# Kernel optimization log

Measured on AMD Instinct MI355X. Metric: run time of the kernel, lower is better.

Reference implementation:

```python
import jax, jax.numpy as jnp
import numpy as np

TOP_K = 2
LN_EPS = 1e-6


def setup_inputs() -> dict:
    key = jax.random.key(0)
    ks = jax.random.split(key, 8)
    B, T, D, FF, E = 4, 512, 1024, 4096, 8
    x = jax.random.normal(ks[0], (B, T, D), dtype=jnp.float32)
    gate_w = jax.random.normal(ks[1], (E, D), dtype=jnp.float32) * (1.0 / np.sqrt(D))
    ln_g = jnp.ones((E, D), dtype=jnp.float32)
    ln_b = jnp.zeros((E, D), dtype=jnp.float32)
    w1 = jax.random.normal(ks[2], (E, FF, D), dtype=jnp.float32) * (1.0 / np.sqrt(D))
    b1 = jnp.zeros((E, FF), dtype=jnp.float32)
    w2 = jax.random.normal(ks[3], (E, D, FF), dtype=jnp.float32) * (1.0 / np.sqrt(FF))
    b2 = jnp.zeros((E, D), dtype=jnp.float32)
    return {"x": x, "gate_w": gate_w, "ln_g": ln_g, "ln_b": ln_b,
            "w1": w1, "b1": b1, "w2": w2, "b2": b2}


def reference(x, gate_w, ln_g, ln_b, w1, b1, w2, b2):
    B, T, D = x.shape
    E = gate_w.shape[0]
    N = B * T
    xf = x.reshape(N, D)

    # ---- Router: linear gate -> softmax -> top-k dispatch mask + aux loss ----
    logits = xf @ gate_w.T                          # [N, E]
    scores = jax.nn.softmax(logits, axis=-1)        # [N, E]
    topk_vals, topk_idx = jax.lax.top_k(scores, TOP_K)
    dispatch = jnp.zeros_like(scores).at[
        jnp.arange(N)[:, None], topk_idx].set(1.0)  # [N, E] 0/1 mask
    load = dispatch.sum(axis=0)                     # [E]
    importance = scores.sum(axis=0)                 # [E]
    aux_loss = (importance * load).sum() * E / (N * N)

    # ---- Experts (PositionwiseFeedForward, kernel_size=1, skip connection) ----
    # Dense-all-experts compute, masked combine: identical math to the
    # per-expert gather/scatter loop in the torch module.
    mu = xf.mean(axis=-1, keepdims=True)
    var = ((xf - mu) ** 2).mean(axis=-1, keepdims=True)
    norm = (xf - mu) / jnp.sqrt(var + LN_EPS)       # [N, D]
    xe = norm[:, None, :] * ln_g[None] + ln_b[None] # [N, E, D] per-expert LN
    h = jax.nn.relu(jnp.einsum('ned,efd->nef', xe, w1) + b1[None])  # [N, E, FF]
    y = jnp.einsum('nef,edf->ned', h, w2) + b2[None] + xf[:, None, :]  # +skip

    comb = scores * dispatch                        # top-k gate weights [N, E]
    out = jnp.einsum('ne,ned->nd', comb, y).reshape(B, T, D)
    return out, aux_loss
```

## Files before the change

kernel.cpp:

```cpp
#include <hip/hip_runtime.h>
#include <hip/hip_bf16.h>

#define N_TOK 2048
#define DMODEL 1024
#define NEXP 8
#define FFDIM 4096
#define NMAX 2048
#define PADROWS 5120
#define TMAX 40

#define BM 128
#define BN 128
#define BK 64
#define KSPL 4

typedef __attribute__((ext_vector_type(8))) short s16x8;
typedef __attribute__((ext_vector_type(4))) float f32x4;

__device__ __forceinline__ float bf2f(ushort u) {
    union { uint i; float f; } x; x.i = ((uint)u) << 16; return x.f;
}
__device__ __forceinline__ ushort f2bf(float f) {
    union { float f; uint i; } x; x.f = f;
    uint r = x.i + 0x7fffu + ((x.i >> 16) & 1u);
    return (ushort)(r >> 16);
}

__device__ __forceinline__ void gl_lds16(const void* g, void* l) {
    __builtin_amdgcn_global_load_lds(
        (const __attribute__((address_space(1))) unsigned int*)g,
        (__attribute__((address_space(3))) unsigned int*)l, 16, 0, 0);
}

__device__ __forceinline__ float block_sum(float v, float* s4) {
    #pragma unroll
    for (int off = 32; off; off >>= 1) v += __shfl_down(v, off);
    __syncthreads();
    if ((threadIdx.x & 63) == 0) s4[threadIdx.x >> 6] = v;
    __syncthreads();
    return s4[0] + s4[1] + s4[2] + s4[3];
}

__global__ __launch_bounds__(256)
void router_kernel(const float* __restrict__ x, const float* __restrict__ gate_w,
                   ushort* __restrict__ norm, float* __restrict__ scores,
                   int* __restrict__ cnt, int* __restrict__ lists,
                   int4* __restrict__ info, float2* __restrict__ gpair) {
    __shared__ float s4[4];
    const int n = blockIdx.x, tid = threadIdx.x;
    const float* xr = x + (size_t)n * DMODEL;
    float4 v = *(const float4*)(xr + tid * 4);

    float tot = block_sum(v.x + v.y + v.z + v.w, s4);
    float mu = tot * (1.0f / DMODEL);
    float d0 = v.x - mu, d1 = v.y - mu, d2 = v.z - mu, d3 = v.w - mu;
    float var = block_sum(d0 * d0 + d1 * d1 + d2 * d2 + d3 * d3, s4) * (1.0f / DMODEL);
    float rstd = rsqrtf(var + 1e-6f);

    ushort nb[4] = { f2bf(d0 * rstd), f2bf(d1 * rstd), f2bf(d2 * rstd), f2bf(d3 * rstd) };
    *(uint2*)(norm + (size_t)n * DMODEL + tid * 4) = *(uint2*)nb;

    float lg[NEXP];
    #pragma unroll
    for (int e = 0; e < NEXP; ++e) {
        float4 g = *(const float4*)(gate_w + (size_t)e * DMODEL + tid * 4);
        lg[e] = v.x * g.x + v.y * g.y + v.z * g.z + v.w * g.w;
    }
    #pragma unroll
    for (int e = 0; e < NEXP; ++e) lg[e] = block_sum(lg[e], s4);

    if (tid == 0) {
        float m = lg[0];
        #pragma unroll
        for (int e = 1; e < NEXP; ++e) m = fmaxf(m, lg[e]);
        float ex[NEXP], Z = 0.f;
        #pragma unroll
        for (int e = 0; e < NEXP; ++e) { ex[e] = expf(lg[e] - m); Z += ex[e]; }
        float inv = 1.0f / Z;
        float sc[NEXP];
        #pragma unroll
        for (int e = 0; e < NEXP; ++e) { sc[e] = ex[e] * inv; scores[n * NEXP + e] = sc[e]; }
        int i1 = 0;
        #pragma unroll
        for (int e = 1; e < NEXP; ++e) if (sc[e] > sc[i1]) i1 = e;
        int i2 = (i1 == 0) ? 1 : 0;
        #pragma unroll
        for (int e = 0; e < NEXP; ++e) if (e != i1 && sc[e] > sc[i2]) i2 = e;
        int s1 = atomicAdd(&cnt[i1], 1);
        lists[i1 * NMAX + s1] = n;
        int s2 = atomicAdd(&cnt[i2], 1);
        lists[i2 * NMAX + s2] = n;
        info[n] = make_int4(i1, s1, i2, s2);
        gpair[n] = make_float2(sc[i1], sc[i2]);
    }
}

__global__ __launch_bounds__(256)
void prep_kernel(const float* __restrict__ scores, const int* __restrict__ cnt,
                 int* __restrict__ offs_pad, int* __restrict__ ntiles,
                 int4* __restrict__ tilemap, float* __restrict__ aux_out) {
    __shared__ float s4[4];
    __shared__ float imp[NEXP];
    float part[NEXP] = {};
    for (int i = threadIdx.x; i < N_TOK; i += 256) {
        #pragma unroll
        for (int e = 0; e < NEXP; ++e) part[e] += scores[i * NEXP + e];
    }
    #pragma unroll
    for (int e = 0; e < NEXP; ++e) {
        float s = block_sum(part[e], s4);
        if (threadIdx.x == 0) imp[e] = s;
    }
    __syncthreads();
    if (threadIdx.x == 0) {
        float aux = 0.f; int pad = 0, idx = 0;
        #pragma unroll
        for (int e = 0; e < NEXP; ++e) {
            aux += imp[e] * (float)cnt[e];
            offs_pad[e] = pad;
            int tiles = (cnt[e] + BM - 1) / BM;
            for (int t = 0; t < tiles; ++t)
                tilemap[idx++] = make_int4(e, pad + t * BM, 0, 0);
            pad += tiles * BM;
        }
        offs_pad[NEXP] = pad;
        ntiles[0] = idx;
        aux_out[0] = aux * (float)NEXP / ((float)N_TOK * (float)N_TOK);
    }
}

__global__ __launch_bounds__(256)
void gather_kernel(const ushort* __restrict__ norm, const float* __restrict__ ln_g,
                   const float* __restrict__ ln_b, const int* __restrict__ offs_pad,
                   const int* __restrict__ cnt, const int* __restrict__ lists,
                   ushort* __restrict__ A1) {
    const int r = blockIdx.x;
    int e = 0;
    #pragma unroll
    for (int k = 1; k < NEXP; ++k) if (r >= offs_pad[k]) e = k;
    const int slot = r - offs_pad[e];
    const int t4 = threadIdx.x * 4;
    if (slot >= cnt[e]) {
        ushort z[4] = {};
        *(uint2*)(A1 + (size_t)r * DMODEL + t4) = *(uint2*)z;
        return;
    }
    const int token = lists[e * NMAX + slot];
    uint2 nbv = *(const uint2*)(norm + (size_t)token * DMODEL + t4);
    ushort ns[4]; *(uint2*)ns = nbv;
    float4 gv = *(const float4*)(ln_g + (size_t)e * DMODEL + t4);
    float4 bv = *(const float4*)(ln_b + (size_t)e * DMODEL + t4);
    ushort ob[4] = { f2bf(bf2f(ns[0]) * gv.x + bv.x), f2bf(bf2f(ns[1]) * gv.y + bv.y),
                     f2bf(bf2f(ns[2]) * gv.z + bv.z), f2bf(bf2f(ns[3]) * gv.w + bv.w) };
    *(uint2*)(A1 + (size_t)r * DMODEL + t4) = *(uint2*)ob;
}

template<int KDIM, int NT, int KSPLT, bool RELU>
__global__ __launch_bounds__(256, 2)
void moe_gemm(const ushort* __restrict__ A, const float* __restrict__ W,
              const float* __restrict__ bias, const int* __restrict__ ntiles,
              const int4* __restrict__ tilemap, ushort* __restrict__ hout,
              float* __restrict__ yout) {
    __shared__ ushort As[2][BM * BK];
    __shared__ ushort Ws[2][BN * BK];
    constexpr int NOUT = NT * BN;

    const int q = (int)gridDim.x >> 3;
    const int logical = ((int)blockIdx.x & 7) * q + ((int)blockIdx.x >> 3);
    const int bt = logical % TMAX;
    int g = logical / TMAX;
    if (bt >= ntiles[0]) return;
    const int nt = g % NT;
    const int kb = g / NT;
    const int4 tm = tilemap[bt];
    const int e = tm.x, row0 = tm.y;

    const int tid = threadIdx.x, lane = tid & 63, wave = tid >> 6;
    const int wm = (wave & 1) * 64, wn = (wave >> 1) * 64;
    const int trow = lane >> 3;
    const int scol = ((lane & 7) ^ trow) * 8;

    const ushort* Agb = A + (size_t)row0 * KDIM;
    const float*  Wgb = W + ((size_t)e * NOUT + nt * BN) * KDIM;

    f32x4 acc[4][4] = {};
    float4 wr[8];

    auto stageA = [&](int step, int b) {
        #pragma unroll
        for (int i = 0; i < 4; ++i) {
            int c = wave * 4 + i;
            gl_lds16(Agb + (size_t)(c * 8 + trow) * KDIM + step * BK + scol, &As[b][c * 512]);
        }
    };
    auto loadWreg = [&](int step) {
        #pragma unroll
        for (int i = 0; i < 4; ++i) {
            int c = tid + 256 * i;
            const float* p = Wgb + (size_t)(c >> 3) * KDIM + step * BK + (c & 7) * 8;
            wr[2 * i]     = *(const float4*)p;
            wr[2 * i + 1] = *(const float4*)(p + 4);
        }
    };
    auto cvtWriteW = [&](int b) {
        #pragma unroll
        for (int i = 0; i < 4; ++i) {
            int c = tid + 256 * i;
            int row = c >> 3, col8 = (c & 7) * 8;
            union { s16x8 v; __hip_bfloat162 h2[4]; } u;
            u.h2[0] = __float22bfloat162_rn(make_float2(wr[2 * i].x, wr[2 * i].y));
            u.h2[1] = __float22bfloat162_rn(make_float2(wr[2 * i].z, wr[2 * i].w));
            u.h2[2] = __float22bfloat162_rn(make_float2(wr[2 * i + 1].x, wr[2 * i + 1].y));
            u.h2[3] = __float22bfloat162_rn(make_float2(wr[2 * i + 1].z, wr[2 * i + 1].w));
            *(s16x8*)&Ws[b][row * BK + (col8 ^ ((row & 7) << 3))] = u.v;
        }
    };
    auto mfma_phase = [&](int b) {
        #pragma unroll
        for (int kki = 0; kki < 2; ++kki) {
            const int cx = (kki * 32 + (lane >> 4) * 8) ^ ((lane & 7) << 3);
            s16x8 af[4], bfv[4];
            #pragma unroll
            for (int mi = 0; mi < 4; ++mi)
                af[mi] = *(const s16x8*)&As[b][(wm + mi * 16 + (lane & 15)) * BK + cx];
            #pragma unroll
            for (int ni = 0; ni < 4; ++ni)
                bfv[ni] = *(const s16x8*)&Ws[b][(wn + ni * 16 + (lane & 15)) * BK + cx];
            #pragma unroll
            for (int mi = 0; mi < 4; ++mi)
                #pragma unroll
                for (int ni = 0; ni < 4; ++ni)
                    acc[mi][ni] = __builtin_amdgcn_mfma_f32_16x16x32_bf16(
                        af[mi], bfv[ni], acc[mi][ni], 0, 0, 0);
        }
    };

    const int KS = KDIM / BK / KSPLT;
    const int kt0 = kb * KS;

    loadWreg(kt0);
    stageA(kt0, 0);
    cvtWriteW(0);
    __syncthreads();

    int buf = 0;
    for (int s = 0; s < KS; ++s) {
        if (s + 1 < KS) {
            stageA(kt0 + s + 1, buf ^ 1);
            loadWreg(kt0 + s + 1);
        }
        mfma_phase(buf);
        if (s + 1 < KS) cvtWriteW(buf ^ 1);
        __syncthreads();
        buf ^= 1;
    }

    if (RELU) {
        #pragma unroll
        for (int ni = 0; ni < 4; ++ni) {
            const int nn = nt * BN + wn + ni * 16 + (lane & 15);
            const float bv = bias[(size_t)e * NOUT + nn];
            #pragma unroll
            for (int mi = 0; mi < 4; ++mi)
                #pragma unroll
                for (int r = 0; r < 4; ++r) {
                    const int sl = wm + mi * 16 + ((lane >> 4) << 2) + r;
                    hout[(size_t)(row0 + sl) * NOUT + nn] =
                        f2bf(fmaxf(acc[mi][ni][r] + bv, 0.f));
                }
        }
    } else {
        #pragma unroll
        for (int ni = 0; ni < 4; ++ni) {
            const int nn = nt * BN + wn + ni * 16 + (lane & 15);
            #pragma unroll
            for (int mi = 0; mi < 4; ++mi)
                #pragma unroll
                for (int r = 0; r < 4; ++r) {
                    const int sl = wm + mi * 16 + ((lane >> 4) << 2) + r;
                    yout[((size_t)kb * PADROWS + row0 + sl) * NOUT + nn] = acc[mi][ni][r];
                }
        }
    }
}

__global__ __launch_bounds__(256)
void combine_kernel(const float* __restrict__ ypart, const float* __restrict__ b2,
                    const float* __restrict__ x, const int* __restrict__ offs_pad,
                    const int4* __restrict__ info, const float2* __restrict__ gpair,
                    float* __restrict__ out) {
    const int n = blockIdx.x, d = threadIdx.x * 4;
    const int4 ii = info[n];
    const float2 g = gpair[n];
    const int r1 = offs_pad[ii.x] + ii.y, r2 = offs_pad[ii.z] + ii.w;
    f32x4 y1 = {}, y2 = {};
    #pragma unroll
    for (int kb = 0; kb < KSPL; ++kb) {
        y1 += *(const f32x4*)(ypart + ((size_t)kb * PADROWS + r1) * DMODEL + d);
        y2 += *(const f32x4*)(ypart + ((size_t)kb * PADROWS + r2) * DMODEL + d);
    }
    const f32x4 b21 = *(const f32x4*)(b2 + (size_t)ii.x * DMODEL + d);
    const f32x4 b22 = *(const f32x4*)(b2 + (size_t)ii.z * DMODEL + d);
    const f32x4 xv  = *(const f32x4*)(x + (size_t)n * DMODEL + d);
    f32x4 o = g.x * (y1 + b21 + xv) + g.y * (y2 + b22 + xv);
    *(f32x4*)(out + (size_t)n * DMODEL + d) = o;
}

extern "C" void kernel_launch(void* const* d_in, const int* in_sizes, int n_in,
                              void* d_out, int out_size, void* d_ws, size_t ws_size,
                              hipStream_t stream) {
    const float* x      = (const float*)d_in[0];
    const float* gate_w = (const float*)d_in[1];
    const float* ln_g   = (const float*)d_in[2];
    const float* ln_b   = (const float*)d_in[3];
    const float* w1     = (const float*)d_in[4];
    const float* b1     = (const float*)d_in[5];
    const float* w2     = (const float*)d_in[6];
    const float* b2     = (const float*)d_in[7];
    float* out = (float*)d_out;

    char* w = (char*)d_ws;
    int*    cnt      = (int*)(w + 0);
    int*    offs_pad = (int*)(w + 64);
    int*    ntiles   = (int*)(w + 128);
    int4*   tilemap  = (int4*)(w + 192);
    int*    lists    = (int*)(w + 1024);
    float*  scores   = (float*)(w + 66560);
    int4*   info     = (int4*)(w + 132096);
    float2* gpair    = (float2*)(w + 164864);
    ushort* norm     = (ushort*)(w + 181248);
    ushort* A1       = (ushort*)(w + 4375552);
    ushort* h        = (ushort*)(w + 14861312);
    float*  ypart    = (float*)(w + 56804352);

    hipMemsetAsync(cnt, 0, 64, stream);

    router_kernel<<<N_TOK, 256, 0, stream>>>(x, gate_w, norm, scores, cnt, lists, info, gpair);
    prep_kernel<<<1, 256, 0, stream>>>(scores, cnt, offs_pad, ntiles, tilemap,
                                       out + (size_t)N_TOK * DMODEL);
    gather_kernel<<<PADROWS, 256, 0, stream>>>(norm, ln_g, ln_b, offs_pad, cnt, lists, A1);
    moe_gemm<DMODEL, FFDIM / BN, 1, true><<<TMAX * (FFDIM / BN), 256, 0, stream>>>(
        A1, w1, b1, ntiles, tilemap, h, nullptr);
    moe_gemm<FFDIM, DMODEL / BN, KSPL, false><<<TMAX * (DMODEL / BN) * KSPL, 256, 0, stream>>>(
        h, w2, nullptr, ntiles, tilemap, nullptr, ypart);
    combine_kernel<<<N_TOK, 256, 0, stream>>>(ypart, b2, x, offs_pad, info, gpair, out);
}
```

Baseline: 309.9 us.

## Drop LDS double buffering and raise occupancy target in MoE GEMM

Replaces the double-buffered LDS pipeline with a single buffer. Each k-step now loads A and W, converts W, syncs, runs the MFMAs and syncs again. Launch bounds go from 2 to 4 blocks per CU, relying on more resident blocks to hide latency instead of in-kernel prefetch. This halves LDS use per block, but it loses load/compute overlap within a block and adds a second barrier per step. The tighter register budget may also cause spills given the 64 fp32 accumulators and W staging registers.

```diff
diff --git a/kernel.cpp b/kernel.cpp
--- a/kernel.cpp
+++ b/kernel.cpp
@@ -156,13 +156,13 @@
 }
 
 template<int KDIM, int NT, int KSPLT, bool RELU>
-__global__ __launch_bounds__(256, 2)
+__global__ __launch_bounds__(256, 4)
 void moe_gemm(const ushort* __restrict__ A, const float* __restrict__ W,
               const float* __restrict__ bias, const int* __restrict__ ntiles,
               const int4* __restrict__ tilemap, ushort* __restrict__ hout,
               float* __restrict__ yout) {
-    __shared__ ushort As[2][BM * BK];
-    __shared__ ushort Ws[2][BN * BK];
+    __shared__ ushort As[BM * BK];
+    __shared__ ushort Ws[BN * BK];
     constexpr int NOUT = NT * BN;
 
     const int q = (int)gridDim.x >> 3;
@@ -186,11 +186,11 @@
     f32x4 acc[4][4] = {};
     float4 wr[8];
 
-    auto stageA = [&](int step, int b) {
+    auto stageA = [&](int step) {
         #pragma unroll
         for (int i = 0; i < 4; ++i) {
             int c = wave * 4 + i;
-            gl_lds16(Agb + (size_t)(c * 8 + trow) * KDIM + step * BK + scol, &As[b][c * 512]);
+            gl_lds16(Agb + (size_t)(c * 8 + trow) * KDIM + step * BK + scol, &As[c * 512]);
         }
     };
     auto loadWreg = [&](int step) {
@@ -202,7 +202,7 @@
             wr[2 * i + 1] = *(const float4*)(p + 4);
         }
     };
-    auto cvtWriteW = [&](int b) {
+    auto cvtWriteW = [&]() {
         #pragma unroll
         for (int i = 0; i < 4; ++i) {
             int c = tid + 256 * i;
@@ -212,20 +212,20 @@
             u.h2[1] = __float22bfloat162_rn(make_float2(wr[2 * i].z, wr[2 * i].w));
             u.h2[2] = __float22bfloat162_rn(make_float2(wr[2 * i + 1].x, wr[2 * i + 1].y));
             u.h2[3] = __float22bfloat162_rn(make_float2(wr[2 * i + 1].z, wr[2 * i + 1].w));
-            *(s16x8*)&Ws[b][row * BK + (col8 ^ ((row & 7) << 3))] = u.v;
+            *(s16x8*)&Ws[row * BK + (col8 ^ ((row & 7) << 3))] = u.v;
         }
     };
-    auto mfma_phase = [&](int b) {
+    auto mfma_phase = [&]() {
         #pragma unroll
         for (int kki = 0; kki < 2; ++kki) {
             const int cx = (kki * 32 + (lane >> 4) * 8) ^ ((lane & 7) << 3);
             s16x8 af[4], bfv[4];
             #pragma unroll
             for (int mi = 0; mi < 4; ++mi)
-                af[mi] = *(const s16x8*)&As[b][(wm + mi * 16 + (lane & 15)) * BK + cx];
+                af[mi] = *(const s16x8*)&As[(wm + mi * 16 + (lane & 15)) * BK + cx];
             #pragma unroll
             for (int ni = 0; ni < 4; ++ni)
-                bfv[ni] = *(const s16x8*)&Ws[b][(wn + ni * 16 + (lane & 15)) * BK + cx];
+                bfv[ni] = *(const s16x8*)&Ws[(wn + ni * 16 + (lane & 15)) * BK + cx];
             #pragma unroll
             for (int mi = 0; mi < 4; ++mi)
                 #pragma unroll
@@ -238,21 +238,13 @@
     const int KS = KDIM / BK / KSPLT;
     const int kt0 = kb * KS;
 
-    loadWreg(kt0);
-    stageA(kt0, 0);
-    cvtWriteW(0);
-    __syncthreads();
-
-    int buf = 0;
     for (int s = 0; s < KS; ++s) {
-        if (s + 1 < KS) {
-            stageA(kt0 + s + 1, buf ^ 1);
-            loadWreg(kt0 + s + 1);
-        }
-        mfma_phase(buf);
-        if (s + 1 < KS) cvtWriteW(buf ^ 1);
+        stageA(kt0 + s);
+        loadWreg(kt0 + s);
+        cvtWriteW();
         __syncthreads();
-        buf ^= 1;
+        mfma_phase();
+        __syncthreads();
     }
 
     if (RELU) {
```

New measurement: 279.0 us. 1.11x faster.
